# Kernel tuning notes

Hardware: AMD Instinct MI355X
Metric: run time of the kernel (lower is better)

## Reference

```python
import jax, jax.numpy as jnp
import numpy as np

B = 16384
D = 64            # bottom_mlp_layers[-1] = embedding_dim
DENSE = 512
HIST = 50         # history length per row
C_CAMP = 1000     # num_collisions for campaign table (sqrt(1e6))
C_FEAT = 316      # num_collisions for 1e5-vocab tables
NQ_CAMP = 1000    # ceil(1e6/1000)
NQ_FEAT = 317     # ceil(1e5/316)
NFEAT = 7
N = NFEAT + 1 + 1 # sparse features + dense row
PROJ = 128


def setup_inputs() -> dict:
    key = jax.random.key(0)
    ks = jax.random.split(key, 20)
    inp = {
        'x': jax.random.normal(ks[0], (B, DENSE), jnp.float32),
        'hist_idx': jax.random.randint(ks[1], (B * HIST,), 0, 1000000),
        'hist_offsets': jnp.arange(B, dtype=jnp.int64) * HIST,
        'feat_idx': jax.random.randint(ks[2], (B, NFEAT), 0, 100000),
        # QR embedding tables (quotient, remainder)
        'Wq_c': jax.random.normal(ks[3], (NQ_CAMP, D), jnp.float32) * 0.05,
        'Wr_c': jax.random.normal(ks[4], (C_CAMP, D), jnp.float32) * 0.05,
        'Wq_f': jax.random.normal(ks[5], (NFEAT, NQ_FEAT, D), jnp.float32) * 0.05,
        'Wr_f': jax.random.normal(ks[6], (NFEAT, C_FEAT, D), jnp.float32) * 0.05,
        # bottom MLP: 512->512 relu 512->256 relu 256->64
        'W0': jax.random.normal(ks[7], (512, DENSE), jnp.float32) * 0.03,
        'b0': jnp.zeros((512,), jnp.float32),
        'W1': jax.random.normal(ks[8], (256, 512), jnp.float32) * 0.04,
        'b1': jnp.zeros((256,), jnp.float32),
        'W2': jax.random.normal(ks[9], (64, 256), jnp.float32) * 0.06,
        'b2': jnp.zeros((64,), jnp.float32),
        # projection: (D + (N^2-N)/2) -> PROJ ; 64 + 36 = 100
        'Wp': jax.random.normal(ks[10], (PROJ, D + (N * N - N) // 2), jnp.float32) * 0.1,
        'bp': jnp.zeros((PROJ,), jnp.float32),
    }
    return inp


def _forward(x, hist_idx, hist_offsets, feat_idx, Wq_c, Wr_c, Wq_f, Wr_f,
             W0, b0, W1, b1, W2, b2, Wp, bp):
    # bottom MLP
    h = jax.nn.relu(x @ W0.T + b0)
    h = jax.nn.relu(h @ W1.T + b1)
    dense = h @ W2.T + b2                                   # [B, D]

    # QR embedding bag (mode='mean', operation='mult') for history feature
    e = Wq_c[hist_idx // C_CAMP] * Wr_c[hist_idx % C_CAMP]  # [M, D]
    M = hist_idx.shape[0]
    seg = jnp.cumsum(jnp.zeros((M,), jnp.int32).at[hist_offsets].add(1)) - 1
    sums = jax.ops.segment_sum(e, seg, num_segments=B)      # [B, D]
    counts = jnp.diff(jnp.concatenate([hist_offsets, jnp.array([M], hist_offsets.dtype)]))
    hist_emb = sums / counts[:, None].astype(sums.dtype)

    # single-valued QR lookups (bag size 1 -> mean == lookup)
    t = jnp.arange(NFEAT)[None, :]
    fe = Wq_f[t, feat_idx // C_FEAT] * Wr_f[t, feat_idx % C_FEAT]  # [B, NFEAT, D]

    # pairwise dot interaction: upper triangle (offset=1) of T @ T^T
    T = jnp.concatenate([dense[:, None, :], hist_emb[:, None, :], fe], axis=1)  # [B, N, D]
    Z = jnp.einsum('bnd,bmd->bnm', T, T)
    row, col = np.triu_indices(N, k=1)
    Z_flat = Z[:, row, col]                                  # [B, (N^2-N)/2]

    combined = jnp.concatenate([dense, Z_flat], axis=1)
    return combined @ Wp.T + bp                              # [B, PROJ]


def reference(x, hist_idx, hist_offsets, feat_idx, Wq_c, Wr_c, Wq_f, Wr_f,
              W0, b0, W1, b1, W2, b2, Wp, bp):
    return _forward(x, hist_idx, hist_offsets, feat_idx, Wq_c, Wr_c, Wq_f, Wr_f,
                    W0, b0, W1, b1, W2, b2, Wp, bp)
```

## Files before the change

kernel.cpp:

```cpp
#include <hip/hip_runtime.h>
#include <hip/hip_bf16.h>
#include <stdint.h>

#define DENSE_D 512
#define HIDDEN1 512
#define HIDDEN2 256
#define EMB_D   64
#define NFEAT   7
#define NROWS   9
#define NPAIRS  36
#define COMB    100
#define KPROJ   128
#define PROJ    128
#define C_CAMP  1000
#define C_FEAT  316
#define NQ_FEAT 317
#define TROWS   16

typedef __attribute__((ext_vector_type(8)))  __bf16 bf16x8;
typedef __attribute__((ext_vector_type(8)))  unsigned short ushort8;
typedef __attribute__((ext_vector_type(4)))  float  facc4;
typedef __attribute__((ext_vector_type(16))) float  facc16;

#define GLD_LDS16(gp, lp) __builtin_amdgcn_global_load_lds( \
    (__attribute__((address_space(1))) void*)(gp), \
    (__attribute__((address_space(3))) void*)(lp), 16, 0, 0)

__device__ inline unsigned short f2bf(float f) {
    __hip_bfloat16 h = __float2bfloat16(f);
    return *reinterpret_cast<unsigned short*>(&h);
}
__device__ inline float blo(unsigned int u) { return __uint_as_float(u << 16); }
__device__ inline float bhi(unsigned int u) { return __uint_as_float(u & 0xffff0000u); }

template<int BM, int BN, int WN, bool RELU, bool OUT_BF16, bool A_F32>
__global__ __launch_bounds__(WN * 64)
void gemm32(const void* __restrict__ Avoid,
            const __hip_bfloat16* __restrict__ W,
            const float* __restrict__ bias,
            void* __restrict__ Cout,
            int M, int N, int K)
{
    constexpr int BK      = 32;
    constexpr int THREADS = WN * 64;
    constexpr int MREP    = BM / 32;
    constexpr int NREP    = BN / (WN * 32);
    constexpr int ACH     = BM * BK / 8;
    constexpr int BCH     = BN * BK / 8;

    __shared__ __align__(16) __hip_bfloat16 Asm[BK / 8][BM][8];
    __shared__ __align__(16) __hip_bfloat16 Bsm[BK / 8][BN][8];

    const int tid  = threadIdx.x;
    const int lane = tid & 63;
    const int wave = tid >> 6;
    const int row0 = blockIdx.x * BM;
    const int col0 = blockIdx.y * BN;
    const int fr   = lane & 31;
    const int fh   = lane >> 5;

    facc16 acc[MREP][NREP] = {};

    for (int k0 = 0; k0 < K; k0 += BK) {
        if (A_F32) {
            const float* Af = (const float*)Avoid;
            for (int p = tid; p < ACH; p += THREADS) {
                const int r  = p & (BM - 1);
                const int kc = p / BM;
                const float* src = Af + (size_t)(row0 + r) * K + k0 + kc * 8;
                const float4 v0 = *reinterpret_cast<const float4*>(src);
                const float4 v1 = *reinterpret_cast<const float4*>(src + 4);
                ushort8 cv;
                cv[0] = f2bf(v0.x); cv[1] = f2bf(v0.y);
                cv[2] = f2bf(v0.z); cv[3] = f2bf(v0.w);
                cv[4] = f2bf(v1.x); cv[5] = f2bf(v1.y);
                cv[6] = f2bf(v1.z); cv[7] = f2bf(v1.w);
                *reinterpret_cast<ushort8*>(
                    (unsigned short*)(&Asm[0][0][0]) + (size_t)p * 8) = cv;
            }
        } else {
            const __hip_bfloat16* Ab = (const __hip_bfloat16*)Avoid;
            for (int p = tid; p < ACH; p += THREADS) {
                const int r  = p & (BM - 1);
                const int kc = p / BM;
                GLD_LDS16(Ab + (size_t)(row0 + r) * K + k0 + kc * 8,
                          (&Asm[0][0][0]) + (size_t)p * 8);
            }
        }
        for (int p = tid; p < BCH; p += THREADS) {
            const int r  = p & (BN - 1);
            const int kc = p / BN;
            GLD_LDS16(W + (size_t)(col0 + r) * K + k0 + kc * 8,
                      (&Bsm[0][0][0]) + (size_t)p * 8);
        }
        __syncthreads();

        bf16x8 af[2][MREP], bw[2][NREP];
        #pragma unroll
        for (int s = 0; s < 2; ++s) {
            #pragma unroll
            for (int m = 0; m < MREP; ++m)
                af[s][m] = *reinterpret_cast<const bf16x8*>(
                    &Asm[s * 2 + fh][m * 32 + fr][0]);
            #pragma unroll
            for (int n = 0; n < NREP; ++n)
                bw[s][n] = *reinterpret_cast<const bf16x8*>(
                    &Bsm[s * 2 + fh][wave * (NREP * 32) + n * 32 + fr][0]);
        }
        #pragma unroll
        for (int s = 0; s < 2; ++s)
            #pragma unroll
            for (int m = 0; m < MREP; ++m)
                #pragma unroll
                for (int n = 0; n < NREP; ++n)
                    acc[m][n] = __builtin_amdgcn_mfma_f32_32x32x16_bf16(
                        af[s][m], bw[s][n], acc[m][n], 0, 0, 0);
        __syncthreads();
    }

    #pragma unroll
    for (int n = 0; n < NREP; ++n) {
        const int col = col0 + wave * (NREP * 32) + n * 32 + fr;
        const float bv = bias[col];
        #pragma unroll
        for (int m = 0; m < MREP; ++m) {
            #pragma unroll
            for (int r = 0; r < 16; ++r) {
                const int row = row0 + m * 32 + (r & 3) + 8 * (r >> 2) + 4 * fh;
                float v = acc[m][n][r] + bv;
                if (RELU) v = fmaxf(v, 0.f);
                if (OUT_BF16)
                    ((__hip_bfloat16*)Cout)[(size_t)row * N + col] = __float2bfloat16(v);
                else
                    ((float*)Cout)[(size_t)row * N + col] = v;
            }
        }
    }
}

__device__ inline void cast_seg(const float* __restrict__ src,
                                unsigned short* __restrict__ dst,
                                int n4, int id, int stride)
{
    for (int i = id; i < n4; i += stride) {
        const float4 v = reinterpret_cast<const float4*>(src)[i];
        ushort4 o;
        o.x = f2bf(v.x); o.y = f2bf(v.y); o.z = f2bf(v.z); o.w = f2bf(v.w);
        reinterpret_cast<ushort4*>(dst)[i] = o;
    }
}

__global__ __launch_bounds__(256)
void prep_all(const float* __restrict__ W0, const float* __restrict__ W1,
              const float* __restrict__ W2, const float* __restrict__ Wp,
              const float* __restrict__ Wq_c, const float* __restrict__ Wr_c,
              const float* __restrict__ Wq_f, const float* __restrict__ Wr_f,
              unsigned short* w0b, unsigned short* w1b, unsigned short* w2b,
              unsigned short* wpb, unsigned short* qcb, unsigned short* rcb,
              unsigned short* qfb, unsigned short* rfb)
{
    const int id = blockIdx.x * blockDim.x + threadIdx.x;
    const int stride = gridDim.x * blockDim.x;
    cast_seg(W0,   w0b, HIDDEN1 * DENSE_D / 4, id, stride);
    cast_seg(W1,   w1b, HIDDEN2 * HIDDEN1 / 4, id, stride);
    cast_seg(W2,   w2b, EMB_D * HIDDEN2 / 4,   id, stride);
    cast_seg(Wq_c, qcb, C_CAMP * EMB_D / 4,    id, stride);
    cast_seg(Wr_c, rcb, C_CAMP * EMB_D / 4,    id, stride);
    cast_seg(Wq_f, qfb, NFEAT * NQ_FEAT * EMB_D / 4, id, stride);
    cast_seg(Wr_f, rfb, NFEAT * C_FEAT * EMB_D / 4,  id, stride);
    for (int i = id; i < PROJ * KPROJ; i += stride) {
        const int r = i >> 7, c = i & 127;
        wpb[i] = (c < COMB) ? f2bf(Wp[r * COMB + c]) : (unsigned short)0;
    }
}

__global__ __launch_bounds__(256)
void tail_fused(const unsigned short* __restrict__ h1b,
                const unsigned short* __restrict__ w2b,
                const float* __restrict__ b2,
                const int* __restrict__ hist_idx,
                const int* __restrict__ hist_off,
                const int* __restrict__ feat_idx,
                const unsigned short* __restrict__ qcb,
                const unsigned short* __restrict__ rcb,
                const unsigned short* __restrict__ qfb,
                const unsigned short* __restrict__ rfb,
                const unsigned short* __restrict__ wpb,
                const float* __restrict__ bp,
                float* __restrict__ out,
                int B, int Mtot)
{
    const int r0   = blockIdx.x * TROWS;
    const int t    = threadIdx.x;
    const int lane = t & 63;
    const int wave = t >> 6;
    const int fr   = lane & 15;
    const int fk   = lane >> 4;

    __shared__ __align__(16) unsigned short T[TROWS][NROWS][68];
    __shared__ __align__(16) unsigned short combs[TROWS][136];

    {
        facc4 acc = {};
        const unsigned short* arow = h1b + (size_t)(r0 + fr) * HIDDEN2;
        const unsigned short* brow = w2b + (size_t)(wave * 16 + fr) * HIDDEN2;
        #pragma unroll
        for (int kw = 0; kw < 8; ++kw) {
            const bf16x8 af = *reinterpret_cast<const bf16x8*>(arow + kw * 32 + fk * 8);
            const bf16x8 bw = *reinterpret_cast<const bf16x8*>(brow + kw * 32 + fk * 8);
            acc = __builtin_amdgcn_mfma_f32_16x16x32_bf16(af, bw, acc, 0, 0, 0);
        }
        const int col = wave * 16 + fr;
        const float bv = b2[col];
        #pragma unroll
        for (int j = 0; j < 4; ++j) {
            const int row = fk * 4 + j;
            const unsigned short hv = f2bf(acc[j] + bv);
            T[row][0][col]  = hv;
            combs[row][col] = hv;
        }
    }

    for (int p = t; p < TROWS * 18; p += 256) {
        const int row = p / 18, c = p % 18;
        *reinterpret_cast<unsigned int*>(&combs[row][100 + c * 2]) = 0u;
    }

    {
        const int row = t >> 4;
        const int oc  = t & 15;
        const int br  = r0 + row;

        const int fbase = br * NFEAT;
        #pragma unroll
        for (int f = 0; f < NFEAT; ++f) {
            const int fi = feat_idx[fbase + f];
            const int q = fi / C_FEAT, r = fi - q * C_FEAT;
            const uint2 qv = *reinterpret_cast<const uint2*>(
                qfb + ((size_t)f * NQ_FEAT + q) * EMB_D + oc * 4);
            const uint2 rv = *reinterpret_cast<const uint2*>(
                rfb + ((size_t)f * C_FEAT + r) * EMB_D + oc * 4);
            union { ushort4 v; uint2 u; } pk;
            pk.v.x = f2bf(blo(qv.x) * blo(rv.x));
            pk.v.y = f2bf(bhi(qv.x) * bhi(rv.x));
            pk.v.z = f2bf(blo(qv.y) * blo(rv.y));
            pk.v.w = f2bf(bhi(qv.y) * bhi(rv.y));
            *reinterpret_cast<uint2*>(&T[row][2 + f][oc * 4]) = pk.u;
        }

        const int start = hist_off[br];
        const int end   = (br + 1 < B) ? hist_off[br + 1] : Mtot;
        const int cnt   = end - start;
        const int* hp = hist_idx + start;
        float a0 = 0.f, a1 = 0.f, a2 = 0.f, a3 = 0.f;
        #pragma unroll 2
        for (int i = 0; i < cnt; ++i) {
            const int hi = hp[i];
            const int q = hi / C_CAMP, r = hi - q * C_CAMP;
            const uint2 qv = *reinterpret_cast<const uint2*>(qcb + (size_t)q * EMB_D + oc * 4);
            const uint2 rv = *reinterpret_cast<const uint2*>(rcb + (size_t)r * EMB_D + oc * 4);
            a0 += blo(qv.x) * blo(rv.x);
            a1 += bhi(qv.x) * bhi(rv.x);
            a2 += blo(qv.y) * blo(rv.y);
            a3 += bhi(qv.y) * bhi(rv.y);
        }
        const float inv = 1.f / (float)max(cnt, 1);
        union { ushort4 v; uint2 u; } pk;
        pk.v.x = f2bf(a0 * inv); pk.v.y = f2bf(a1 * inv);
        pk.v.z = f2bf(a2 * inv); pk.v.w = f2bf(a3 * inv);
        *reinterpret_cast<uint2*>(&T[row][1][oc * 4]) = pk.u;
    }
    __syncthreads();

    for (int p = t; p < NPAIRS * TROWS; p += 256) {
        const int row = p & (TROWS - 1);
        const int pr  = p / TROWS;
        int i = 0, rem = pr;
        while (rem >= (NROWS - 1) - i) { rem -= (NROWS - 1) - i; ++i; }
        const int j = i + 1 + rem;
        const unsigned short* ti = &T[row][i][0];
        const unsigned short* tj = &T[row][j][0];
        float s = 0.f;
        #pragma unroll
        for (int d = 0; d < EMB_D; d += 4) {
            const uint2 u = *reinterpret_cast<const uint2*>(ti + d);
            const uint2 v = *reinterpret_cast<const uint2*>(tj + d);
            s += blo(u.x) * blo(v.x) + bhi(u.x) * bhi(v.x)
               + blo(u.y) * blo(v.y) + bhi(u.y) * bhi(v.y);
        }
        combs[row][EMB_D + pr] = f2bf(s);
    }
    __syncthreads();

    {
        facc4 acc[2] = {};
        #pragma unroll
        for (int kw = 0; kw < 4; ++kw) {
            const bf16x8 af = *reinterpret_cast<const bf16x8*>(
                &combs[fr][kw * 32 + fk * 8]);
            #pragma unroll
            for (int n = 0; n < 2; ++n) {
                const bf16x8 bw = *reinterpret_cast<const bf16x8*>(
                    wpb + (size_t)(wave * 32 + n * 16 + fr) * KPROJ + kw * 32 + fk * 8);
                acc[n] = __builtin_amdgcn_mfma_f32_16x16x32_bf16(af, bw, acc[n], 0, 0, 0);
            }
        }
        #pragma unroll
        for (int n = 0; n < 2; ++n) {
            const int col = wave * 32 + n * 16 + fr;
            const float bv = bp[col];
            #pragma unroll
            for (int j = 0; j < 4; ++j) {
                const int row = fk * 4 + j;
                out[(size_t)(r0 + row) * PROJ + col] = acc[n][j] + bv;
            }
        }
    }
}

extern "C" void kernel_launch(void* const* d_in, const int* in_sizes, int n_in,
                              void* d_out, int out_size, void* d_ws, size_t ws_size,
                              hipStream_t stream)
{
    const float* x        = (const float*)d_in[0];
    const int*   hist_idx = (const int*)  d_in[1];
    const int*   hist_off = (const int*)  d_in[2];
    const int*   feat_idx = (const int*)  d_in[3];
    const float* Wq_c     = (const float*)d_in[4];
    const float* Wr_c     = (const float*)d_in[5];
    const float* Wq_f     = (const float*)d_in[6];
    const float* Wr_f     = (const float*)d_in[7];
    const float* W0       = (const float*)d_in[8];
    const float* b0       = (const float*)d_in[9];
    const float* W1       = (const float*)d_in[10];
    const float* b1       = (const float*)d_in[11];
    const float* W2       = (const float*)d_in[12];
    const float* b2       = (const float*)d_in[13];
    const float* Wp       = (const float*)d_in[14];
    const float* bp       = (const float*)d_in[15];

    const int M    = in_sizes[0] / DENSE_D;
    const int Mtot = in_sizes[1];

    char* w = (char*)d_ws;
    auto take = [&](size_t bytes) { char* p = w; w += (bytes + 255) & ~(size_t)255; return p; };
    unsigned short* w0b = (unsigned short*)take(HIDDEN1 * DENSE_D * 2);
    unsigned short* w1b = (unsigned short*)take(HIDDEN2 * HIDDEN1 * 2);
    unsigned short* w2b = (unsigned short*)take(EMB_D * HIDDEN2 * 2);
    unsigned short* wpb = (unsigned short*)take(PROJ * KPROJ * 2);
    unsigned short* qcb = (unsigned short*)take(C_CAMP * EMB_D * 2);
    unsigned short* rcb = (unsigned short*)take(C_CAMP * EMB_D * 2);
    unsigned short* qfb = (unsigned short*)take(NFEAT * NQ_FEAT * EMB_D * 2);
    unsigned short* rfb = (unsigned short*)take(NFEAT * C_FEAT * EMB_D * 2);
    unsigned short* h0b = (unsigned short*)take((size_t)M * HIDDEN1 * 2);
    unsigned short* h1b = (unsigned short*)take((size_t)M * HIDDEN2 * 2);

    prep_all<<<512, 256, 0, stream>>>(W0, W1, W2, Wp, Wq_c, Wr_c, Wq_f, Wr_f,
                                      w0b, w1b, w2b, wpb, qcb, rcb, qfb, rfb);

    gemm32<64, 512, 8, true, true, true>
        <<<dim3(M / 64, 1), 512, 0, stream>>>(
        x, (const __hip_bfloat16*)w0b, b0, h0b, M, HIDDEN1, DENSE_D);

    gemm32<64, 256, 8, true, true, false>
        <<<dim3(M / 64, 1), 512, 0, stream>>>(
        h0b, (const __hip_bfloat16*)w1b, b1, h1b, M, HIDDEN2, HIDDEN1);

    tail_fused<<<M / TROWS, 256, 0, stream>>>(
        h1b, w2b, b2, hist_idx, hist_off, feat_idx,
        qcb, rcb, qfb, rfb, wpb, bp, (float*)d_out, M, Mtot);
}
```

Baseline: 98.58 us.

## Retile MLP GEMMs to 16x16x32 MFMA with smaller tiles, pre-cast x to bf16

The two bottom-MLP GEMMs move from the 32x32x16 MFMA with 64x512 tiles and 512 threads to 16x16x32 MFMA with 64x128 tiles, BK=64 and 256 threads, using a 2D grid over N. The fp32 input x is now cast to bf16 in the prep kernel, so the first GEMM can load A through direct global-to-LDS loads instead of converting in registers. This gives more blocks for occupancy and removes in-loop conversion. The cost is an extra full write and read of x as bf16, and A tiles that are re-fetched by every N-block.

```diff
diff --git a/kernel.cpp b/kernel.cpp
--- a/kernel.cpp
+++ b/kernel.cpp
@@ -20,7 +20,6 @@
 typedef __attribute__((ext_vector_type(8)))  __bf16 bf16x8;
 typedef __attribute__((ext_vector_type(8)))  unsigned short ushort8;
 typedef __attribute__((ext_vector_type(4)))  float  facc4;
-typedef __attribute__((ext_vector_type(16))) float  facc16;
 
 #define GLD_LDS16(gp, lp) __builtin_amdgcn_global_load_lds( \
     (__attribute__((address_space(1))) void*)(gp), \
@@ -33,61 +32,46 @@
 __device__ inline float blo(unsigned int u) { return __uint_as_float(u << 16); }
 __device__ inline float bhi(unsigned int u) { return __uint_as_float(u & 0xffff0000u); }
 
-template<int BM, int BN, int WN, bool RELU, bool OUT_BF16, bool A_F32>
-__global__ __launch_bounds__(WN * 64)
-void gemm32(const void* __restrict__ Avoid,
-            const __hip_bfloat16* __restrict__ W,
+template<int BM, int BN, int BK, bool RELU>
+__global__ __launch_bounds__(256)
+void gemm16(const unsigned short* __restrict__ A,
+            const unsigned short* __restrict__ W,
             const float* __restrict__ bias,
-            void* __restrict__ Cout,
+            unsigned short* __restrict__ Cout,
             int M, int N, int K)
 {
-    constexpr int BK      = 32;
-    constexpr int THREADS = WN * 64;
-    constexpr int MREP    = BM / 32;
-    constexpr int NREP    = BN / (WN * 32);
+    constexpr int THREADS = 256;
+    constexpr int MREP    = BM / 16;
+    constexpr int NREP    = BN / (4 * 16);
+    constexpr int SUB     = BK / 32;
     constexpr int ACH     = BM * BK / 8;
     constexpr int BCH     = BN * BK / 8;
 
-    __shared__ __align__(16) __hip_bfloat16 Asm[BK / 8][BM][8];
-    __shared__ __align__(16) __hip_bfloat16 Bsm[BK / 8][BN][8];
+    __shared__ __align__(16) unsigned short Asm[BK / 8][BM][8];
+    __shared__ __align__(16) unsigned short Bsm[BK / 8][BN][8];
 
     const int tid  = threadIdx.x;
     const int lane = tid & 63;
     const int wave = tid >> 6;
     const int row0 = blockIdx.x * BM;
     const int col0 = blockIdx.y * BN;
-    const int fr   = lane & 31;
-    const int fh   = lane >> 5;
-
-    facc16 acc[MREP][NREP] = {};
+    const int fr   = lane & 15;
+    const int fk   = lane >> 4;
+
+    facc4 acc[MREP][NREP] = {};
 
     for (int k0 = 0; k0 < K; k0 += BK) {
-        if (A_F32) {
-            const float* Af = (const float*)Avoid;
-            for (int p = tid; p < ACH; p += THREADS) {
-                const int r  = p & (BM - 1);
-                const int kc = p / BM;
-                const float* src = Af + (size_t)(row0 + r) * K + k0 + kc * 8;
-                const float4 v0 = *reinterpret_cast<const float4*>(src);
-                const float4 v1 = *reinterpret_cast<const float4*>(src + 4);
-                ushort8 cv;
-                cv[0] = f2bf(v0.x); cv[1] = f2bf(v0.y);
-                cv[2] = f2bf(v0.z); cv[3] = f2bf(v0.w);
-                cv[4] = f2bf(v1.x); cv[5] = f2bf(v1.y);
-                cv[6] = f2bf(v1.z); cv[7] = f2bf(v1.w);
-                *reinterpret_cast<ushort8*>(
-                    (unsigned short*)(&Asm[0][0][0]) + (size_t)p * 8) = cv;
-            }
-        } else {
-            const __hip_bfloat16* Ab = (const __hip_bfloat16*)Avoid;
-            for (int p = tid; p < ACH; p += THREADS) {
-                const int r  = p & (BM - 1);
-                const int kc = p / BM;
-                GLD_LDS16(Ab + (size_t)(row0 + r) * K + k0 + kc * 8,
-                          (&Asm[0][0][0]) + (size_t)p * 8);
-            }
-        }
-        for (int p = tid; p < BCH; p += THREADS) {
+        #pragma unroll
+        for (int it = 0; it < ACH / THREADS; ++it) {
+            const int p  = it * THREADS + tid;
+            const int r  = p & (BM - 1);
+            const int kc = p / BM;
+            GLD_LDS16(A + (size_t)(row0 + r) * K + k0 + kc * 8,
+                      (&Asm[0][0][0]) + (size_t)p * 8);
+        }
+        #pragma unroll
+        for (int it = 0; it < BCH / THREADS; ++it) {
+            const int p  = it * THREADS + tid;
             const int r  = p & (BN - 1);
             const int kc = p / BN;
             GLD_LDS16(W + (size_t)(col0 + r) * K + k0 + kc * 8,
@@ -95,44 +79,39 @@
         }
         __syncthreads();
 
-        bf16x8 af[2][MREP], bw[2][NREP];
-        #pragma unroll
-        for (int s = 0; s < 2; ++s) {
+        #pragma unroll
+        for (int s = 0; s < SUB; ++s) {
+            bf16x8 af[MREP], bw[NREP];
             #pragma unroll
             for (int m = 0; m < MREP; ++m)
-                af[s][m] = *reinterpret_cast<const bf16x8*>(
-                    &Asm[s * 2 + fh][m * 32 + fr][0]);
+                af[m] = *reinterpret_cast<const bf16x8*>(
+                    &Asm[s * 4 + fk][m * 16 + fr][0]);
             #pragma unroll
             for (int n = 0; n < NREP; ++n)
-                bw[s][n] = *reinterpret_cast<const bf16x8*>(
-                    &Bsm[s * 2 + fh][wave * (NREP * 32) + n * 32 + fr][0]);
-        }
-        #pragma unroll
-        for (int s = 0; s < 2; ++s)
+                bw[n] = *reinterpret_cast<const bf16x8*>(
+                    &Bsm[s * 4 + fk][wave * (NREP * 16) + n * 16 + fr][0]);
             #pragma unroll
             for (int m = 0; m < MREP; ++m)
                 #pragma unroll
                 for (int n = 0; n < NREP; ++n)
-                    acc[m][n] = __builtin_amdgcn_mfma_f32_32x32x16_bf16(
-                        af[s][m], bw[s][n], acc[m][n], 0, 0, 0);
+                    acc[m][n] = __builtin_amdgcn_mfma_f32_16x16x32_bf16(
+                        af[m], bw[n], acc[m][n], 0, 0, 0);
+        }
         __syncthreads();
     }
 
     #pragma unroll
     for (int n = 0; n < NREP; ++n) {
-        const int col = col0 + wave * (NREP * 32) + n * 32 + fr;
+        const int col = col0 + wave * (NREP * 16) + n * 16 + fr;
         const float bv = bias[col];
         #pragma unroll
         for (int m = 0; m < MREP; ++m) {
             #pragma unroll
-            for (int r = 0; r < 16; ++r) {
-                const int row = row0 + m * 32 + (r & 3) + 8 * (r >> 2) + 4 * fh;
-                float v = acc[m][n][r] + bv;
+            for (int j = 0; j < 4; ++j) {
+                const int row = row0 + m * 16 + fk * 4 + j;
+                float v = acc[m][n][j] + bv;
                 if (RELU) v = fmaxf(v, 0.f);
-                if (OUT_BF16)
-                    ((__hip_bfloat16*)Cout)[(size_t)row * N + col] = __float2bfloat16(v);
-                else
-                    ((float*)Cout)[(size_t)row * N + col] = v;
+                Cout[(size_t)row * N + col] = f2bf(v);
             }
         }
     }
@@ -151,21 +130,24 @@
 }
 
 __global__ __launch_bounds__(256)
-void prep_all(const float* __restrict__ W0, const float* __restrict__ W1,
+void prep_all(const float* __restrict__ x,
+              const float* __restrict__ W0, const float* __restrict__ W1,
               const float* __restrict__ W2, const float* __restrict__ Wp,
               const float* __restrict__ Wq_c, const float* __restrict__ Wr_c,
               const float* __restrict__ Wq_f, const float* __restrict__ Wr_f,
+              unsigned short* xb,
               unsigned short* w0b, unsigned short* w1b, unsigned short* w2b,
               unsigned short* wpb, unsigned short* qcb, unsigned short* rcb,
-              unsigned short* qfb, unsigned short* rfb)
+              unsigned short* qfb, unsigned short* rfb, int M)
 {
     const int id = blockIdx.x * blockDim.x + threadIdx.x;
     const int stride = gridDim.x * blockDim.x;
-    cast_seg(W0,   w0b, HIDDEN1 * DENSE_D / 4, id, stride);
-    cast_seg(W1,   w1b, HIDDEN2 * HIDDEN1 / 4, id, stride);
-    cast_seg(W2,   w2b, EMB_D * HIDDEN2 / 4,   id, stride);
-    cast_seg(Wq_c, qcb, C_CAMP * EMB_D / 4,    id, stride);
-    cast_seg(Wr_c, rcb, C_CAMP * EMB_D / 4,    id, stride);
+    cast_seg(x,    xb,  M * DENSE_D / 4,         id, stride);
+    cast_seg(W0,   w0b, HIDDEN1 * DENSE_D / 4,   id, stride);
+    cast_seg(W1,   w1b, HIDDEN2 * HIDDEN1 / 4,   id, stride);
+    cast_seg(W2,   w2b, EMB_D * HIDDEN2 / 4,     id, stride);
+    cast_seg(Wq_c, qcb, C_CAMP * EMB_D / 4,      id, stride);
+    cast_seg(Wr_c, rcb, C_CAMP * EMB_D / 4,      id, stride);
     cast_seg(Wq_f, qfb, NFEAT * NQ_FEAT * EMB_D / 4, id, stride);
     cast_seg(Wr_f, rfb, NFEAT * C_FEAT * EMB_D / 4,  id, stride);
     for (int i = id; i < PROJ * KPROJ; i += stride) {
@@ -344,6 +326,7 @@
 
     char* w = (char*)d_ws;
     auto take = [&](size_t bytes) { char* p = w; w += (bytes + 255) & ~(size_t)255; return p; };
+    unsigned short* xb  = (unsigned short*)take((size_t)M * DENSE_D * 2);
     unsigned short* w0b = (unsigned short*)take(HIDDEN1 * DENSE_D * 2);
     unsigned short* w1b = (unsigned short*)take(HIDDEN2 * HIDDEN1 * 2);
     unsigned short* w2b = (unsigned short*)take(EMB_D * HIDDEN2 * 2);
@@ -355,16 +338,14 @@
     unsigned short* h0b = (unsigned short*)take((size_t)M * HIDDEN1 * 2);
     unsigned short* h1b = (unsigned short*)take((size_t)M * HIDDEN2 * 2);
 
-    prep_all<<<512, 256, 0, stream>>>(W0, W1, W2, Wp, Wq_c, Wr_c, Wq_f, Wr_f,
-                                      w0b, w1b, w2b, wpb, qcb, rcb, qfb, rfb);
-
-    gemm32<64, 512, 8, true, true, true>
-        <<<dim3(M / 64, 1), 512, 0, stream>>>(
-        x, (const __hip_bfloat16*)w0b, b0, h0b, M, HIDDEN1, DENSE_D);
-
-    gemm32<64, 256, 8, true, true, false>
-        <<<dim3(M / 64, 1), 512, 0, stream>>>(
-        h0b, (const __hip_bfloat16*)w1b, b1, h1b, M, HIDDEN2, HIDDEN1);
+    prep_all<<<2048, 256, 0, stream>>>(x, W0, W1, W2, Wp, Wq_c, Wr_c, Wq_f, Wr_f,
+                                       xb, w0b, w1b, w2b, wpb, qcb, rcb, qfb, rfb, M);
+
+    gemm16<64, 128, 64, true><<<dim3(M / 64, HIDDEN1 / 128), 256, 0, stream>>>(
+        xb, w0b, b0, h0b, M, HIDDEN1, DENSE_D);
+
+    gemm16<64, 128, 64, true><<<dim3(M / 64, HIDDEN2 / 128), 256, 0, stream>>>(
+        h0b, w1b, b1, h1b, M, HIDDEN2, HIDDEN1);
 
     tail_fused<<<M / TROWS, 256, 0, stream>>>(
         h1b, w2b, b2, hist_idx, hist_off, feat_idx,
```

Measured after the change: 93.61 us. 1.05x faster.
